# Kernel optimization log

Hardware: AMD Instinct MI355X
Metric: run time of the kernel (lower is better)

## Reference

```python
import jax, jax.numpy as jnp
import numpy as np

NUM_USR = 8192
H = 256  # NUM_SOURCE == H (feature dim of y_a); NUM_TARGET = 256


def setup_inputs() -> dict:
    key = jax.random.key(0)
    k1, k2, k3, k4 = jax.random.split(key, 4)
    return {
        "y_a": jax.random.normal(k1, (NUM_USR, H), dtype=jnp.float32),
        "y_b": jax.random.normal(k2, (NUM_USR, H), dtype=jnp.float32),
        "W": jax.random.normal(k3, (H, H), dtype=jnp.float32) * (1.0 / np.sqrt(H)),
        "b": jax.random.normal(k4, (H,), dtype=jnp.float32) * 0.01,
    }


def reference(y_a, y_b, W, b):
    # Linear: proj[j] = W @ y_b[j] + b   (torch nn.Linear convention)
    proj = jnp.einsum("jt,st->js", y_b, W) + b          # [num_usr, H]
    # torch loop computes score[i, j] = y_a[i] . proj[j], replicated H times
    # then averaged: out[i, k] = (1/H) * sum_j sigmoid(score[i, j])
    scores = jnp.einsum("ih,jh->ij", y_a, proj)          # [num_usr, num_usr]
    s = jnp.sum(jax.nn.sigmoid(scores), axis=1) / y_a.shape[1]  # [num_usr]
    return jnp.broadcast_to(s[:, None], y_a.shape)       # [num_usr, H]
```

## Files before the change

### kernel.cpp

```cpp
#include <hip/hip_runtime.h>

#define NUSR 8192
#define HDIM 256

typedef __attribute__((ext_vector_type(8))) __bf16 bf16x8;
typedef __attribute__((ext_vector_type(4))) float f32x4;

union frag_u { bf16x8 v; unsigned short u[8]; unsigned int d[4]; };

__device__ __forceinline__ unsigned int f2bf(float f) {
  unsigned u = __builtin_bit_cast(unsigned, f);
  u += 0x7FFFu + ((u >> 16) & 1u);
  return u >> 16;
}
__device__ __forceinline__ unsigned int f2bf2(float lo, float hi) {
  return f2bf(lo) | (f2bf(hi) << 16);
}
__device__ __forceinline__ float sigmoidf_fast(float x) {
  float e = __builtin_amdgcn_exp2f(x * -1.44269504088896340736f);
  return __builtin_amdgcn_rcpf(1.0f + e);
}


__global__ __launch_bounds__(256) void k0_prep(
    const float* __restrict__ ya, const float* __restrict__ W,
    unsigned short* __restrict__ yabf, unsigned short* __restrict__ WX,
    float* __restrict__ svec)
{
  const int gid = blockIdx.x * 256 + threadIdx.x;

  {
    const float4* src = (const float4*)ya;
    uint4* dst = (uint4*)yabf;
#pragma unroll
    for (int u = 0; u < 16; ++u) {
      int d = u * 16384 + gid;
      float4 a = src[d * 2];
      float4 b = src[d * 2 + 1];
      uint4 o = { f2bf2(a.x, a.y), f2bf2(a.z, a.w),
                  f2bf2(b.x, b.y), f2bf2(b.z, b.w) };
      dst[d] = o;
    }
  }

  if (gid < 8192) {
    int st = gid >> 9;
    int kb = (gid >> 6) & 7;
    int l  = gid & 63;
    int i  = l & 15, q = l >> 4;
    const float* wr = W + (size_t)(st * 16 + i) * HDIM + kb * 32 + q * 8;
    float4 w0 = *(const float4*)wr;
    float4 w1 = *(const float4*)(wr + 4);
    uint4 o = { f2bf2(w0.x, w0.y), f2bf2(w0.z, w0.w),
                f2bf2(w1.x, w1.y), f2bf2(w1.z, w1.w) };
    *(uint4*)(WX + (size_t)gid * 8) = o;
  }

  if (gid < 8192) svec[gid] = 0.f;
}

__global__ __launch_bounds__(256) void k1_proj(
    const float* __restrict__ yb, const unsigned short* __restrict__ WX,
    const float* __restrict__ bvec, unsigned short* __restrict__ PX)
{
  const int tid  = threadIdx.x;
  const int lane = tid & 63;
  const int w    = tid >> 6;
  const int q    = lane >> 4;
  const int i    = lane & 15;
  const int wid  = blockIdx.x * 4 + w;
  const int jg   = wid >> 2;
  const int qtr  = wid & 3;

  frag_u B[8];
  {
    const float* ybrow = yb + (size_t)(jg * 16 + i) * HDIM;
#pragma unroll
    for (int kb = 0; kb < 8; ++kb) {
      float4 v0 = *(const float4*)&ybrow[kb * 32 + q * 8];
      float4 v1 = *(const float4*)&ybrow[kb * 32 + q * 8 + 4];
      B[kb].d[0] = f2bf2(v0.x, v0.y); B[kb].d[1] = f2bf2(v0.z, v0.w);
      B[kb].d[2] = f2bf2(v1.x, v1.y); B[kb].d[3] = f2bf2(v1.z, v1.w);
    }
  }

#pragma unroll
  for (int t = 0; t < 4; ++t) {
    const int st = qtr * 4 + t;
    f32x4 acc = {0.f, 0.f, 0.f, 0.f};
#pragma unroll
    for (int kb = 0; kb < 8; ++kb) {
      frag_u Af;
      Af.v = *(const bf16x8*)&WX[(size_t)(st * 8 + kb) * 512 + lane * 8];
      acc = __builtin_amdgcn_mfma_f32_16x16x32_bf16(Af.v, B[kb].v, acc, 0, 0, 0);
    }
    float4 bias = *(const float4*)&bvec[st * 16 + q * 4];
    unsigned v0 = f2bf2(acc[0] + bias.x, acc[1] + bias.y);
    unsigned v1 = f2bf2(acc[2] + bias.z, acc[3] + bias.w);
    size_t off = (size_t)jg * 4096 + (size_t)(st >> 1) * 512
               + (size_t)(((st & 1) << 1) | (q >> 1)) * 128 + i * 8 + ((q & 1) * 4);
    *(uint2*)(PX + off) = make_uint2(v0, v1);
  }
}

__global__ __launch_bounds__(256, 2) void k2_score(
    const unsigned short* __restrict__ yabf, const unsigned short* __restrict__ PX,
    float* __restrict__ svec)
{
  __shared__ __align__(16) unsigned short bs[2][8192];
  const int tid  = threadIdx.x;
  const int lane = tid & 63;
  const int w    = tid >> 6;
  const int quad = lane >> 4;
  const int l15  = lane & 15;
  const int rbase = blockIdx.x * 256 + w * 64;
  const int cg16  = blockIdx.y * 32;

  frag_u A[4][8];
#pragma unroll
  for (int g = 0; g < 4; ++g) {
    const unsigned short* src = yabf + (size_t)(rbase + g * 16 + l15) * HDIM;
#pragma unroll
    for (int kb = 0; kb < 8; ++kb)
      A[g][kb].v = *(const bf16x8*)&src[kb * 32 + quad * 8];
  }

  const unsigned short* psrc = PX + (size_t)cg16 * 4096;

  float rs[4][4] = {{0.f,0.f,0.f,0.f},{0.f,0.f,0.f,0.f},
                    {0.f,0.f,0.f,0.f},{0.f,0.f,0.f,0.f}};

#pragma unroll
  for (int p = 0; p < 4; ++p) {
    int c = p * 256 + tid;
    __builtin_amdgcn_global_load_lds(
        (const __attribute__((address_space(1))) unsigned int*)(const void*)(psrc + c * 8),
        (__attribute__((address_space(3))) unsigned int*)(void*)(&bs[0][0] + c * 8),
        16, 0, 0);
  }
  __syncthreads();

  for (int t = 0; t < 16; ++t) {
    if (t < 15) {
      const unsigned short* src = psrc + (size_t)(t + 1) * 8192;
      unsigned short* dst = &bs[(t + 1) & 1][0];
#pragma unroll
      for (int p = 0; p < 4; ++p) {
        int c = p * 256 + tid;
        __builtin_amdgcn_global_load_lds(
            (const __attribute__((address_space(1))) unsigned int*)(const void*)(src + c * 8),
            (__attribute__((address_space(3))) unsigned int*)(void*)(dst + c * 8),
            16, 0, 0);
      }
    }
    const unsigned short* buf = &bs[t & 1][0];
#pragma unroll
    for (int tt = 0; tt < 2; ++tt) {
      f32x4 acc[4] = {{0.f,0.f,0.f,0.f},{0.f,0.f,0.f,0.f},
                      {0.f,0.f,0.f,0.f},{0.f,0.f,0.f,0.f}};
#pragma unroll
      for (int kb = 0; kb < 8; ++kb) {
        bf16x8 bfrag = *(const bf16x8*)&buf[(tt * 512 + kb * 64 + lane) * 8];
#pragma unroll
        for (int g = 0; g < 4; ++g)
          acc[g] = __builtin_amdgcn_mfma_f32_16x16x32_bf16(A[g][kb].v, bfrag, acc[g], 0, 0, 0);
      }
#pragma unroll
      for (int g = 0; g < 4; ++g)
#pragma unroll
        for (int r = 0; r < 4; ++r)
          rs[g][r] += sigmoidf_fast(acc[g][r]);
    }
    __syncthreads();
  }

#pragma unroll
  for (int off = 1; off < 16; off <<= 1)
#pragma unroll
    for (int g = 0; g < 4; ++g)
#pragma unroll
      for (int r = 0; r < 4; ++r)
        rs[g][r] += __shfl_xor(rs[g][r], off, 64);

  if (l15 == 0) {
#pragma unroll
    for (int g = 0; g < 4; ++g)
#pragma unroll
      for (int r = 0; r < 4; ++r)
        atomicAdd(&svec[rbase + g * 16 + quad * 4 + r], rs[g][r]);
  }
}

__global__ __launch_bounds__(256) void k3_bcast(
    const float* __restrict__ svec, float* __restrict__ out)
{
  int idx = blockIdx.x * 256 + threadIdx.x;
  int row = idx >> 6;
  float v = svec[row] * (1.0f / 256.0f);
  float4 o = {v, v, v, v};
  ((float4*)out)[idx] = o;
}

extern "C" void kernel_launch(void* const* d_in, const int* in_sizes, int n_in,
                              void* d_out, int out_size, void* d_ws, size_t ws_size,
                              hipStream_t stream) {
  (void)in_sizes; (void)n_in; (void)out_size;
  const float* ya = (const float*)d_in[0];
  const float* yb = (const float*)d_in[1];
  const float* W  = (const float*)d_in[2];
  const float* bv = (const float*)d_in[3];
  float* out = (float*)d_out;

  char* ws = (char*)d_ws;
  unsigned short *PX, *yabf, *WX;
  float* svec;
  const size_t need = (8ull << 20) + (256ull << 10);
  if (ws_size >= need) {
    PX   = (unsigned short*)ws;
    yabf = (unsigned short*)(ws + (4 << 20));
    WX   = (unsigned short*)(ws + (8 << 20));
    svec = (float*)(ws + (8 << 20) + (128 << 10));
  } else {
    PX   = (unsigned short*)d_out;
    yabf = (unsigned short*)((char*)d_out + (4 << 20));
    WX   = (unsigned short*)ws;
    svec = (float*)(ws + (128 << 10));
  }

  k0_prep<<<64, 256, 0, stream>>>(ya, W, yabf, WX, svec);
  k1_proj<<<512, 256, 0, stream>>>(yb, WX, bv, PX);
  k2_score<<<dim3(32, 16), 256, 0, stream>>>(yabf, PX, svec);
  k3_bcast<<<2048, 256, 0, stream>>>(svec, out);
}
```

Baseline: 118.5 us.

## Fuse prep and projection kernels, and fold broadcast into score tail

Merges the bf16 conversion of y_a, the W conversion and the projection into one kernel. Projection blocks now convert W on the fly and each wave computes four row groups, so the W fragment is reused across them. The final broadcast is folded into the score kernel: the last block to finish each row tile, found with a per-tile atomic counter, writes the averaged outputs. This removes two kernel launches and the WX intermediate, at the cost of redundant W conversion per block and an atomic completion protocol.

```diff
diff --git a/kernel.cpp b/kernel.cpp
--- a/kernel.cpp
+++ b/kernel.cpp
@@ -22,92 +22,94 @@
 }
 
 
-__global__ __launch_bounds__(256) void k0_prep(
-    const float* __restrict__ ya, const float* __restrict__ W,
-    unsigned short* __restrict__ yabf, unsigned short* __restrict__ WX,
-    float* __restrict__ svec)
+__global__ __launch_bounds__(256) void k1_fused(
+    const float* __restrict__ ya, const float* __restrict__ yb,
+    const float* __restrict__ W, const float* __restrict__ bvec,
+    unsigned short* __restrict__ yabf, unsigned short* __restrict__ PX,
+    float* __restrict__ svec, unsigned int* __restrict__ done)
 {
-  const int gid = blockIdx.x * 256 + threadIdx.x;
-
-  {
+  const int b   = blockIdx.x;
+  const int tid = threadIdx.x;
+
+  if (b < 128) {
+    const int lane = tid & 63;
+    const int w    = tid >> 6;
+    const int q    = lane >> 4;
+    const int i    = lane & 15;
+
+    frag_u B[4][8];
+#pragma unroll
+    for (int g = 0; g < 4; ++g) {
+      const float* ybrow = yb + (size_t)(b * 64 + g * 16 + i) * HDIM;
+#pragma unroll
+      for (int kb = 0; kb < 8; ++kb) {
+        float4 v0 = *(const float4*)&ybrow[kb * 32 + q * 8];
+        float4 v1 = *(const float4*)&ybrow[kb * 32 + q * 8 + 4];
+        B[g][kb].d[0] = f2bf2(v0.x, v0.y); B[g][kb].d[1] = f2bf2(v0.z, v0.w);
+        B[g][kb].d[2] = f2bf2(v1.x, v1.y); B[g][kb].d[3] = f2bf2(v1.z, v1.w);
+      }
+    }
+
+#pragma unroll
+    for (int t = 0; t < 4; ++t) {
+      const int st = w * 4 + t;
+      f32x4 acc[4] = {{0.f,0.f,0.f,0.f},{0.f,0.f,0.f,0.f},
+                      {0.f,0.f,0.f,0.f},{0.f,0.f,0.f,0.f}};
+#pragma unroll
+      for (int kb = 0; kb < 8; ++kb) {
+        const float* wr = W + (size_t)(st * 16 + i) * HDIM + kb * 32 + q * 8;
+        float4 w0 = *(const float4*)wr;
+        float4 w1 = *(const float4*)(wr + 4);
+        frag_u Af;
+        Af.d[0] = f2bf2(w0.x, w0.y); Af.d[1] = f2bf2(w0.z, w0.w);
+        Af.d[2] = f2bf2(w1.x, w1.y); Af.d[3] = f2bf2(w1.z, w1.w);
+#pragma unroll
+        for (int g = 0; g < 4; ++g)
+          acc[g] = __builtin_amdgcn_mfma_f32_16x16x32_bf16(Af.v, B[g][kb].v, acc[g], 0, 0, 0);
+      }
+      float4 bias = *(const float4*)&bvec[st * 16 + q * 4];
+#pragma unroll
+      for (int g = 0; g < 4; ++g) {
+        const int jg = b * 4 + g;
+        unsigned v0 = f2bf2(acc[g][0] + bias.x, acc[g][1] + bias.y);
+        unsigned v1 = f2bf2(acc[g][2] + bias.z, acc[g][3] + bias.w);
+        size_t off = (size_t)jg * 4096 + (size_t)(st >> 1) * 512
+                   + (size_t)(((st & 1) << 1) | (q >> 1)) * 128 + i * 8 + ((q & 1) * 4);
+        *(uint2*)(PX + off) = make_uint2(v0, v1);
+      }
+    }
+  } else {
+    const int id = (b - 128) * 256 + tid;
     const float4* src = (const float4*)ya;
     uint4* dst = (uint4*)yabf;
 #pragma unroll
-    for (int u = 0; u < 16; ++u) {
-      int d = u * 16384 + gid;
-      float4 a = src[d * 2];
-      float4 b = src[d * 2 + 1];
-      uint4 o = { f2bf2(a.x, a.y), f2bf2(a.z, a.w),
-                  f2bf2(b.x, b.y), f2bf2(b.z, b.w) };
-      dst[d] = o;
-    }
-  }
-
-  if (gid < 8192) {
-    int st = gid >> 9;
-    int kb = (gid >> 6) & 7;
-    int l  = gid & 63;
-    int i  = l & 15, q = l >> 4;
-    const float* wr = W + (size_t)(st * 16 + i) * HDIM + kb * 32 + q * 8;
-    float4 w0 = *(const float4*)wr;
-    float4 w1 = *(const float4*)(wr + 4);
-    uint4 o = { f2bf2(w0.x, w0.y), f2bf2(w0.z, w0.w),
-                f2bf2(w1.x, w1.y), f2bf2(w1.z, w1.w) };
-    *(uint4*)(WX + (size_t)gid * 8) = o;
-  }
-
-  if (gid < 8192) svec[gid] = 0.f;
-}
-
-__global__ __launch_bounds__(256) void k1_proj(
-    const float* __restrict__ yb, const unsigned short* __restrict__ WX,
-    const float* __restrict__ bvec, unsigned short* __restrict__ PX)
-{
-  const int tid  = threadIdx.x;
-  const int lane = tid & 63;
-  const int w    = tid >> 6;
-  const int q    = lane >> 4;
-  const int i    = lane & 15;
-  const int wid  = blockIdx.x * 4 + w;
-  const int jg   = wid >> 2;
-  const int qtr  = wid & 3;
-
-  frag_u B[8];
-  {
-    const float* ybrow = yb + (size_t)(jg * 16 + i) * HDIM;
-#pragma unroll
-    for (int kb = 0; kb < 8; ++kb) {
-      float4 v0 = *(const float4*)&ybrow[kb * 32 + q * 8];
-      float4 v1 = *(const float4*)&ybrow[kb * 32 + q * 8 + 4];
-      B[kb].d[0] = f2bf2(v0.x, v0.y); B[kb].d[1] = f2bf2(v0.z, v0.w);
-      B[kb].d[2] = f2bf2(v1.x, v1.y); B[kb].d[3] = f2bf2(v1.z, v1.w);
-    }
-  }
-
-#pragma unroll
-  for (int t = 0; t < 4; ++t) {
-    const int st = qtr * 4 + t;
-    f32x4 acc = {0.f, 0.f, 0.f, 0.f};
-#pragma unroll
-    for (int kb = 0; kb < 8; ++kb) {
-      frag_u Af;
-      Af.v = *(const bf16x8*)&WX[(size_t)(st * 8 + kb) * 512 + lane * 8];
-      acc = __builtin_amdgcn_mfma_f32_16x16x32_bf16(Af.v, B[kb].v, acc, 0, 0, 0);
-    }
-    float4 bias = *(const float4*)&bvec[st * 16 + q * 4];
-    unsigned v0 = f2bf2(acc[0] + bias.x, acc[1] + bias.y);
-    unsigned v1 = f2bf2(acc[2] + bias.z, acc[3] + bias.w);
-    size_t off = (size_t)jg * 4096 + (size_t)(st >> 1) * 512
-               + (size_t)(((st & 1) << 1) | (q >> 1)) * 128 + i * 8 + ((q & 1) * 4);
-    *(uint2*)(PX + off) = make_uint2(v0, v1);
+    for (int u = 0; u < 3; ++u) {
+      int d = id + u * 98304;
+      if (d < 262144) {
+        float4 a = src[d * 2];
+        float4 c = src[d * 2 + 1];
+        uint4 o = { f2bf2(a.x, a.y), f2bf2(a.z, a.w),
+                    f2bf2(c.x, c.y), f2bf2(c.z, c.w) };
+        dst[d] = o;
+      }
+    }
+    if (b == 511) {
+      float4 z = {0.f, 0.f, 0.f, 0.f};
+      float4* sv = (float4*)svec;
+#pragma unroll
+      for (int u = 0; u < 8; ++u) sv[u * 256 + tid] = z;
+      if (tid < 32) done[tid] = 0u;
+    }
   }
 }
 
 __global__ __launch_bounds__(256, 2) void k2_score(
     const unsigned short* __restrict__ yabf, const unsigned short* __restrict__ PX,
-    float* __restrict__ svec)
+    float* __restrict__ svec, unsigned int* __restrict__ done,
+    float* __restrict__ out, const int fuse_tail)
 {
   __shared__ __align__(16) unsigned short bs[2][8192];
+  __shared__ unsigned int lastv;
   const int tid  = threadIdx.x;
   const int lane = tid & 63;
   const int w    = tid >> 6;
@@ -188,6 +190,27 @@
 #pragma unroll
       for (int r = 0; r < 4; ++r)
         atomicAdd(&svec[rbase + g * 16 + quad * 4 + r], rs[g][r]);
+  }
+
+  if (!fuse_tail) return;
+
+  __syncthreads();
+  if (tid == 0)
+    lastv = __hip_atomic_fetch_add(&done[blockIdx.x], 1u,
+                                   __ATOMIC_ACQ_REL, __HIP_MEMORY_SCOPE_AGENT);
+  __syncthreads();
+  if (lastv == 15u) {
+    const int rb = blockIdx.x * 256;
+    const float inv = 1.0f / 256.0f;
+#pragma unroll 4
+    for (int u = 0; u < 64; ++u) {
+      int row = u * 4 + w;
+      float s = __hip_atomic_load(&svec[rb + row],
+                                  __ATOMIC_RELAXED, __HIP_MEMORY_SCOPE_AGENT);
+      float v = s * inv;
+      float4 o = {v, v, v, v};
+      ((float4*)out)[(size_t)(rb + row) * 64 + lane] = o;
+    }
   }
 }
 
@@ -212,23 +235,26 @@
   float* out = (float*)d_out;
 
   char* ws = (char*)d_ws;
-  unsigned short *PX, *yabf, *WX;
+  unsigned short *PX, *yabf;
   float* svec;
-  const size_t need = (8ull << 20) + (256ull << 10);
+  unsigned int* done;
+  int fuse;
+  const size_t need = (8ull << 20) + (64ull << 10);
   if (ws_size >= need) {
     PX   = (unsigned short*)ws;
     yabf = (unsigned short*)(ws + (4 << 20));
-    WX   = (unsigned short*)(ws + (8 << 20));
-    svec = (float*)(ws + (8 << 20) + (128 << 10));
+    svec = (float*)(ws + (8 << 20));
+    done = (unsigned int*)(ws + (8 << 20) + (32 << 10));
+    fuse = 1;
   } else {
     PX   = (unsigned short*)d_out;
     yabf = (unsigned short*)((char*)d_out + (4 << 20));
-    WX   = (unsigned short*)ws;
-    svec = (float*)(ws + (128 << 10));
-  }
-
-  k0_prep<<<64, 256, 0, stream>>>(ya, W, yabf, WX, svec);
-  k1_proj<<<512, 256, 0, stream>>>(yb, WX, bv, PX);
-  k2_score<<<dim3(32, 16), 256, 0, stream>>>(yabf, PX, svec);
-  k3_bcast<<<2048, 256, 0, stream>>>(svec, out);
-}
+    svec = (float*)ws;
+    done = (unsigned int*)(ws + (32 << 10));
+    fuse = 0;
+  }
+
+  k1_fused<<<512, 256, 0, stream>>>(ya, yb, W, bv, yabf, PX, svec, done);
+  k2_score<<<dim3(32, 16), 256, 0, stream>>>(yabf, PX, svec, done, out, fuse);
+  if (!fuse) k3_bcast<<<2048, 256, 0, stream>>>(svec, out);
+}
```

Result: slower. 138.7 us (+17.0%).
